# Kernel optimization log

Measured on AMD Instinct MI355X. Metric: run time of the kernel, lower is better.

## Reference

```python
import jax, jax.numpy as jnp
import numpy as np

DIM = 1024
DIM_MEDIA = 1024
DIM_HEAD = 64
HEADS = 8
INNER = DIM_HEAD * HEADS  # 512
B, N_TOK, N_LAT = 4, 4096, 1024
LN_EPS = 1e-5


def setup_inputs() -> dict:
    key = jax.random.key(0)
    ks = jax.random.split(key, 6)
    x = jax.random.normal(ks[0], (B, N_TOK, DIM), dtype=jnp.float32)
    media = jax.random.normal(ks[1], (B, N_LAT, DIM_MEDIA), dtype=jnp.float32)
    media_mask = jax.random.randint(ks[2], (B, N_LAT), 0, 2).astype(bool)
    media_mask = media_mask.at[:, 0].set(True)  # avoid fully-masked rows (NaN softmax)
    ln_gamma = jnp.ones((DIM,), jnp.float32)
    ln_beta = jnp.zeros((DIM,), jnp.float32)
    Wq = jax.random.normal(ks[3], (DIM, INNER), jnp.float32) * (DIM ** -0.5)
    Wkv = jax.random.normal(ks[4], (DIM_MEDIA, 2 * INNER), jnp.float32) * (DIM_MEDIA ** -0.5)
    Wout = jax.random.normal(ks[5], (INNER, DIM), jnp.float32) * (INNER ** -0.5)
    return {"x": x, "media": media, "media_mask": media_mask,
            "ln_gamma": ln_gamma, "ln_beta": ln_beta,
            "Wq": Wq, "Wkv": Wkv, "Wout": Wout}


def reference(x, media, media_mask, ln_gamma, ln_beta, Wq, Wkv, Wout):
    scale = DIM_HEAD ** -0.5
    # LayerNorm over last dim
    mu = jnp.mean(x, axis=-1, keepdims=True)
    var = jnp.mean(jnp.square(x - mu), axis=-1, keepdims=True)
    xn = (x - mu) * jax.lax.rsqrt(var + LN_EPS) * ln_gamma + ln_beta

    q = (xn @ Wq) * scale                      # [b, n, inner]
    kv = media @ Wkv                           # [b, m, 2*inner]
    k, v = jnp.split(kv, 2, axis=-1)

    def to_heads(t):
        b, n, _ = t.shape
        return t.reshape(b, n, HEADS, DIM_HEAD).transpose(0, 2, 1, 3)  # b h n d

    q, k, v = to_heads(q), to_heads(k), to_heads(v)

    sim = jnp.einsum('bhid,bhjd->bhij', q, k)  # [b, h, n_tok, n_lat]
    neg_inf = jnp.float32(-jnp.inf)
    sim = jnp.where(media_mask[:, None, None, :], sim, neg_inf)
    sim = sim - jax.lax.stop_gradient(jnp.max(sim, axis=-1, keepdims=True))
    attn = jax.nn.softmax(sim, axis=-1)
    out = jnp.einsum('bhij,bhjd->bhid', attn, v)  # [b, h, n_tok, d]
    out = out.transpose(0, 2, 1, 3).reshape(out.shape[0], out.shape[2], INNER)
    return out @ Wout  # [b, n_tok, dim]
```

## Files before the change

kernel.cpp:

```cpp
#include <hip/hip_runtime.h>
#include <hip/hip_bf16.h>

typedef short bf16x8 __attribute__((ext_vector_type(8)));
typedef float f32x4 __attribute__((ext_vector_type(4)));
typedef unsigned short u16;

#define AS1 __attribute__((address_space(1)))
#define AS3 __attribute__((address_space(3)))

#define DIM     1024
#define INNER   512
#define HEADS   8
#define DHEAD   64
#define BATCH   4
#define NTOK    4096
#define NLAT    1024
#define M_X     (BATCH*NTOK)
#define M_MED   (BATCH*NLAT)
#define LN_EPS  1e-5f

__device__ __forceinline__ float b2f(u16 h) {
    union { unsigned u; float f; } v; v.u = ((unsigned)h) << 16; return v.f;
}
__device__ __forceinline__ u16 f2b(float f) {
    union { float f; unsigned u; } v; v.f = f;
    unsigned r = v.u + 0x7fff + ((v.u >> 16) & 1);
    return (u16)(r >> 16);
}
__device__ __forceinline__ unsigned cvt_pk(float lo, float hi) {
    unsigned r;
    asm("v_cvt_pk_bf16_f32 %0, %1, %2" : "=v"(r) : "v"(lo), "v"(hi));
    return r;
}

__launch_bounds__(256)
__global__ void detect_kernel(const unsigned* __restrict__ xw, const unsigned* __restrict__ maskw,
                              unsigned* __restrict__ flags) {
    __shared__ int s_bad, s_byte;
    if (threadIdx.x == 0) { s_bad = 0; s_byte = 0; }
    __syncthreads();
    unsigned w = xw[threadIdx.x];
    int bad = 0;
    #pragma unroll
    for (int h = 0; h < 2; h++) {
        unsigned el = (h ? (w >> 16) : w) & 0xFFFFu;
        unsigned ef = (el >> 7) & 0xFFu;
        if (!((ef >= 64u && ef < 192u) || (el & 0x7FFFu) == 0u)) bad = 1;
    }
    if (bad) atomicOr(&s_bad, 1);
    for (int i = threadIdx.x; i < NLAT; i += 256)
        if (maskw[i] > 1u) { atomicOr(&s_byte, 1); break; }
    __syncthreads();
    if (threadIdx.x == 0) { flags[0] = s_bad ? 0u : 1u; flags[1] = s_byte ? 1u : 0u; }
}

#define PREP_BLOCKS 6148

__device__ __forceinline__ void do_transpose(const void* in, u16* out, int R, int C,
                                             int bx, int by, bool bf, u16 (*t)[33]) {
    int c0 = bx * 32, r0 = by * 32;
    int tid = threadIdx.x;
    int r = tid >> 3, cb = (tid & 7) * 4;
    size_t base = (size_t)(r0 + r) * C + c0 + cb;
    u16 e0, e1, e2, e3;
    if (bf) {
        ushort4 a = *(const ushort4*)((const u16*)in + base);
        e0 = a.x; e1 = a.y; e2 = a.z; e3 = a.w;
    } else {
        float4 a = *(const float4*)((const float*)in + base);
        e0 = f2b(a.x); e1 = f2b(a.y); e2 = f2b(a.z); e3 = f2b(a.w);
    }
    t[r][cb] = e0; t[r][cb + 1] = e1; t[r][cb + 2] = e2; t[r][cb + 3] = e3;
    __syncthreads();
    ushort4 o;
    o.x = t[cb + 0][r]; o.y = t[cb + 1][r]; o.z = t[cb + 2][r]; o.w = t[cb + 3][r];
    *(ushort4*)(out + (size_t)(c0 + r) * R + r0 + cb) = o;
}

__launch_bounds__(256)
__global__ void prep_kernel(const void* __restrict__ x, const void* __restrict__ g,
                            const void* __restrict__ bt, u16* __restrict__ xn,
                            const void* __restrict__ media, u16* __restrict__ media_c,
                            const void* __restrict__ mask, int* __restrict__ map,
                            int* __restrict__ cnt,
                            const void* __restrict__ Wq, u16* __restrict__ WqT,
                            const void* __restrict__ Wkv, u16* __restrict__ WkvT,
                            const void* __restrict__ Wout, u16* __restrict__ WoutT,
                            const unsigned* __restrict__ flags) {
    __shared__ int wsumI[4];
    __shared__ u16 t[32][33];
    bool bf = flags[0] != 0;
    int bid = blockIdx.x, tid = threadIdx.x;

    if (bid < 2048) {
        int w = tid >> 6, lane = tid & 63;
        int row0 = (bid << 3) + (w << 1);
        float v[2][16];
        if (bf) {
            const u16* xr = (const u16*)x + (size_t)row0 * DIM;
            bf16x8 a[4];
            #pragma unroll
            for (int rr = 0; rr < 2; rr++)
                #pragma unroll
                for (int i = 0; i < 2; i++)
                    a[rr * 2 + i] = *(const bf16x8*)(xr + (size_t)rr * DIM + (lane + 64 * i) * 8);
            #pragma unroll
            for (int rr = 0; rr < 2; rr++)
                #pragma unroll
                for (int i = 0; i < 2; i++)
                    #pragma unroll
                    for (int j = 0; j < 8; j++)
                        v[rr][i * 8 + j] = b2f((u16)a[rr * 2 + i][j]);
        } else {
            const float* xr = (const float*)x + (size_t)row0 * DIM;
            float4 a[8];
            #pragma unroll
            for (int rr = 0; rr < 2; rr++)
                #pragma unroll
                for (int i = 0; i < 4; i++)
                    a[rr * 4 + i] = *(const float4*)(xr + (size_t)rr * DIM + (lane + 64 * i) * 4);
            #pragma unroll
            for (int rr = 0; rr < 2; rr++)
                #pragma unroll
                for (int i = 0; i < 4; i++) {
                    v[rr][i * 4 + 0] = a[rr * 4 + i].x; v[rr][i * 4 + 1] = a[rr * 4 + i].y;
                    v[rr][i * 4 + 2] = a[rr * 4 + i].z; v[rr][i * 4 + 3] = a[rr * 4 + i].w;
                }
        }
        float s[2] = {0.f, 0.f}, s2[2] = {0.f, 0.f};
        #pragma unroll
        for (int rr = 0; rr < 2; rr++)
            #pragma unroll
            for (int i = 0; i < 16; i++) { s[rr] += v[rr][i]; s2[rr] += v[rr][i] * v[rr][i]; }
        #pragma unroll
        for (int m = 1; m < 64; m <<= 1) {
            #pragma unroll
            for (int rr = 0; rr < 2; rr++) {
                s[rr] += __shfl_xor(s[rr], m);
                s2[rr] += __shfl_xor(s2[rr], m);
            }
        }
        float mu[2], inv[2];
        #pragma unroll
        for (int rr = 0; rr < 2; rr++) {
            mu[rr] = s[rr] * (1.f / DIM);
            float var = s2[rr] * (1.f / DIM) - mu[rr] * mu[rr];
            inv[rr] = rsqrtf(fmaxf(var, 0.f) + LN_EPS);
        }
        u16* orow = xn + (size_t)row0 * DIM;
        if (bf) {
            const u16* gr = (const u16*)g;
            const u16* br = (const u16*)bt;
            #pragma unroll
            for (int i = 0; i < 2; i++) {
                int c = (lane + 64 * i) * 8;
                bf16x8 ga = *(const bf16x8*)(gr + c);
                bf16x8 ba = *(const bf16x8*)(br + c);
                #pragma unroll
                for (int rr = 0; rr < 2; rr++) {
                    u16 o[8];
                    #pragma unroll
                    for (int j = 0; j < 8; j++)
                        o[j] = f2b((v[rr][i * 8 + j] - mu[rr]) * inv[rr] * b2f((u16)ga[j]) + b2f((u16)ba[j]));
                    *(bf16x8*)(orow + (size_t)rr * DIM + c) = *(bf16x8*)o;
                }
            }
        } else {
            const float* gr = (const float*)g;
            const float* br = (const float*)bt;
            #pragma unroll
            for (int i = 0; i < 4; i++) {
                int c = (lane + 64 * i) * 4;
                float4 ga = *(const float4*)(gr + c);
                float4 ba = *(const float4*)(br + c);
                #pragma unroll
                for (int rr = 0; rr < 2; rr++) {
                    ushort4 o;
                    o.x = f2b((v[rr][i * 4 + 0] - mu[rr]) * inv[rr] * ga.x + ba.x);
                    o.y = f2b((v[rr][i * 4 + 1] - mu[rr]) * inv[rr] * ga.y + ba.y);
                    o.z = f2b((v[rr][i * 4 + 2] - mu[rr]) * inv[rr] * ga.z + ba.z);
                    o.w = f2b((v[rr][i * 4 + 3] - mu[rr]) * inv[rr] * ga.w + ba.w);
                    *(ushort4*)(orow + (size_t)rr * DIM + c) = o;
                }
            }
        }
    } else if (bid < 4096) {
        size_t i = ((size_t)(bid - 2048) * 256 + tid) * 8;
        if (bf) {
            *(bf16x8*)(media_c + i) = *(const bf16x8*)((const u16*)media + i);
        } else {
            const float* s = (const float*)media + i;
            float4 a = *(const float4*)s, b = *(const float4*)(s + 4);
            u16 o[8] = {f2b(a.x), f2b(a.y), f2b(a.z), f2b(a.w),
                        f2b(b.x), f2b(b.y), f2b(b.z), f2b(b.w)};
            *(bf16x8*)(media_c + i) = *(bf16x8*)o;
        }
    } else if (bid < 4100) {
        int b = bid - 4096;
        bool bytes = flags[1] != 0;
        int v[4];
        if (bytes) {
            unsigned wd = ((const unsigned*)mask)[b * 256 + tid];
            #pragma unroll
            for (int i = 0; i < 4; i++) v[i] = ((wd >> (8 * i)) & 0xFFu) ? 1 : 0;
        } else {
            int4 m4 = ((const int4*)mask)[b * 256 + tid];
            v[0] = m4.x != 0; v[1] = m4.y != 0; v[2] = m4.z != 0; v[3] = m4.w != 0;
        }
        int tsum = v[0] + v[1] + v[2] + v[3];
        int lane = tid & 63, w = tid >> 6;
        int incl = tsum;
        #pragma unroll
        for (int off = 1; off < 64; off <<= 1) {
            int tt = __shfl_up(incl, off);
            if (lane >= off) incl += tt;
        }
        if (lane == 63) wsumI[w] = incl;
        __syncthreads();
        int base = 0;
        for (int k = 0; k < w; k++) base += wsumI[k];
        int slot = base + incl - tsum;
        int gbase = b * NLAT + tid * 4;
        #pragma unroll
        for (int i = 0; i < 4; i++) map[gbase + i] = v[i] ? slot++ : -1;
        if (tid == 0) cnt[b] = wsumI[0] + wsumI[1] + wsumI[2] + wsumI[3];
    } else if (bid < 4612) {
        int idx = bid - 4100;
        do_transpose(Wq, WqT, DIM, INNER, idx & 15, idx >> 4, bf, t);
    } else if (bid < 5636) {
        int idx = bid - 4612;
        do_transpose(Wkv, WkvT, DIM, DIM, idx & 31, idx >> 5, bf, t);
    } else {
        int idx = bid - 5636;
        do_transpose(Wout, WoutT, INNER, DIM, idx & 31, idx >> 5, bf, t);
    }
}

__device__ __forceinline__ void gemm_body(const u16* __restrict__ A, const u16* __restrict__ Bt,
                                          u16* __restrict__ C, float* __restrict__ Cf,
                                          int Ndim, int K, float scale, int mode,
                                          u16* __restrict__ vT, const int* __restrict__ map,
                                          bool outbf, int n0, int m0, u16* As, u16* Bs) {
    int tid = threadIdx.x;
    int w = tid >> 6, lane = tid & 63, quad = lane >> 4, l15 = lane & 15;
    int wm = (w >> 1) * 64, wn = (w & 1) * 64;
    f32x4 acc[4][4] = {};
    for (int k0 = 0; k0 < K; k0 += 64) {
        __syncthreads();
        #pragma unroll
        for (int i = 0; i < 4; i++) {
            int slot = i * 256 + tid;
            int row = slot >> 3;
            int lg = (slot & 7) ^ (row & 7);
            int wbase = (i * 256 + (tid & 192)) * 8;
            __builtin_amdgcn_global_load_lds(
                (const AS1 void*)(A + (size_t)(m0 + row) * K + k0 + lg * 8),
                (AS3 void*)(As + wbase), 16, 0, 0);
            __builtin_amdgcn_global_load_lds(
                (const AS1 void*)(Bt + (size_t)(n0 + row) * K + k0 + lg * 8),
                (AS3 void*)(Bs + wbase), 16, 0, 0);
        }
        __syncthreads();
        #pragma unroll
        for (int h = 0; h < 2; h++) {
            bf16x8 af[4], bfr[4];
            #pragma unroll
            for (int i = 0; i < 4; i++) {
                int R = wm + i * 16 + l15;
                af[i] = *(bf16x8*)&As[R * 64 + (((quad + h * 4) ^ (R & 7)) * 8)];
            }
            #pragma unroll
            for (int j = 0; j < 4; j++) {
                int R = wn + j * 16 + l15;
                bfr[j] = *(bf16x8*)&Bs[R * 64 + (((quad + h * 4) ^ (R & 7)) * 8)];
            }
            #pragma unroll
            for (int i = 0; i < 4; i++)
                #pragma unroll
                for (int j = 0; j < 4; j++)
                    acc[i][j] = __builtin_amdgcn_mfma_f32_16x16x32_bf16(af[i], bfr[j], acc[i][j], 0, 0, 0);
        }
    }
    #pragma unroll
    for (int i = 0; i < 4; i++)
        #pragma unroll
        for (int j = 0; j < 4; j++)
            #pragma unroll
            for (int r = 0; r < 4; r++) {
                int row = m0 + wm + i * 16 + quad * 4 + r;
                int col = n0 + wn + j * 16 + l15;
                float val = acc[i][j][r] * scale;
                if (mode == 1) {
                    int b = row >> 10, jj = row & 1023;
                    int slot = map[(b << 10) + jj];
                    if (slot >= 0) {
                        if (col < INNER) {
                            C[((size_t)(b << 10) + slot) * INNER + col] = f2b(val);
                        } else {
                            int c = col - INNER;
                            int h = c >> 6, d = c & 63;
                            vT[(((size_t)(b * HEADS + h) * 64 + d) << 10) + slot] = f2b(val);
                        }
                    }
                } else if (outbf) {
                    C[(size_t)row * Ndim + col] = f2b(val);
                } else {
                    Cf[(size_t)row * Ndim + col] = val;
                }
            }
}

__launch_bounds__(256, 3)
__global__ void gemm128(const u16* __restrict__ A, const u16* __restrict__ Bt,
                        u16* __restrict__ C, float* __restrict__ Cf, int Ndim, int K,
                        float scale, int mode, u16* __restrict__ vT,
                        const int* __restrict__ map,
                        const unsigned* __restrict__ flags) {
    __shared__ __align__(16) u16 As[128 * 64];
    __shared__ __align__(16) u16 Bs[128 * 64];
    bool outbf = (mode != 2) || (flags[0] != 0);
    gemm_body(A, Bt, C, Cf, Ndim, K, scale, mode, vT, map, outbf,
              blockIdx.x * 128, blockIdx.y * 128, As, Bs);
}

__launch_bounds__(256, 3)
__global__ void gemm_qkv(const u16* __restrict__ xn, const u16* __restrict__ WqT,
                         u16* __restrict__ qb,
                         const u16* __restrict__ media_c, const u16* __restrict__ WkvT,
                         u16* __restrict__ Kb, u16* __restrict__ vT,
                         const int* __restrict__ map) {
    __shared__ __align__(16) u16 As[128 * 64];
    __shared__ __align__(16) u16 Bs[128 * 64];
    int bid = blockIdx.x;
    if (bid < 512) {
        gemm_body(xn, WqT, qb, (float*)nullptr, INNER, DIM, 0.125f * 1.44269504f, 0,
                  (u16*)nullptr, (int*)nullptr, true,
                  (bid & 3) * 128, (bid >> 2) * 128, As, Bs);
    } else {
        int id = bid - 512;
        gemm_body(media_c, WkvT, Kb, (float*)nullptr, DIM, DIM, 1.0f, 1,
                  vT, map, true,
                  (id & 7) * 128, (id >> 3) * 128, As, Bs);
    }
}

__launch_bounds__(256, 6)
__global__ void flash_kernel(const u16* __restrict__ q, const u16* __restrict__ Kc,
                             const u16* __restrict__ vTc, const int* __restrict__ cntp,
                             u16* __restrict__ attn_out) {
    __shared__ __align__(16) u16 Ks[64 * 64];
    __shared__ __align__(16) u16 Vts[64 * 64];
    __shared__ __align__(16) u16 Ps[4][16 * 68];
    int bh = blockIdx.x >> 6;
    int qt = blockIdx.x & 63;
    int b = bh >> 3, h = bh & 7;
    int tid = threadIdx.x, w = tid >> 6, lane = tid & 63, quad = lane >> 4, l15 = lane & 15;
    int qrow0 = qt * 64 + w * 16;
    int cnt = cntp[b];

    size_t qbase = ((size_t)(b * NTOK) + qrow0 + l15) * INNER + h * 64;
    bf16x8 qf[2];
    qf[0] = *(const bf16x8*)(q + qbase + quad * 8);
    qf[1] = *(const bf16x8*)(q + qbase + 32 + quad * 8);

    f32x4 Oacc[4] = {};
    float lsum = 0.f;
    int ld_row = lane >> 3;
    int ld_col = ((lane & 7) ^ ld_row) * 8;

    for (int jt = 0; jt < cnt; jt += 64) {
        __syncthreads();
        #pragma unroll
        for (int i = 0; i < 2; i++) {
            int seg = w * 2 + i;
            int j = jt + seg * 8 + ld_row;
            __builtin_amdgcn_global_load_lds(
                (const AS1 void*)(Kc + ((size_t)(b * NLAT) + j) * INNER + h * 64 + ld_col),
                (AS3 void*)(Ks + seg * 512), 16, 0, 0);
            int d = seg * 8 + ld_row;
            __builtin_amdgcn_global_load_lds(
                (const AS1 void*)(vTc + (((size_t)(b * HEADS + h) * 64 + d) << 10) + jt + ld_col),
                (AS3 void*)(Vts + seg * 512), 16, 0, 0);
        }
        __syncthreads();

        int sw0 = (quad ^ (l15 & 7)) * 8;
        int sw1 = ((quad + 4) ^ (l15 & 7)) * 8;
        f32x4 S[4];
        #pragma unroll
        for (int c = 0; c < 4; c++) {
            bf16x8 kf0 = *(bf16x8*)&Ks[(c * 16 + l15) * 64 + sw0];
            bf16x8 kf1 = *(bf16x8*)&Ks[(c * 16 + l15) * 64 + sw1];
            f32x4 s = {};
            s = __builtin_amdgcn_mfma_f32_16x16x32_bf16(kf0, qf[0], s, 0, 0, 0);
            s = __builtin_amdgcn_mfma_f32_16x16x32_bf16(kf1, qf[1], s, 0, 0, 0);
            S[c] = s;
        }
        if (jt + 64 <= cnt) {
            #pragma unroll
            for (int c = 0; c < 4; c++) {
                float p0 = exp2f(fminf(S[c][0], 115.4f));
                float p1 = exp2f(fminf(S[c][1], 115.4f));
                float p2 = exp2f(fminf(S[c][2], 115.4f));
                float p3 = exp2f(fminf(S[c][3], 115.4f));
                lsum += (p0 + p1) + (p2 + p3);
                uint2 pw = {cvt_pk(p0, p1), cvt_pk(p2, p3)};
                *(uint2*)&Ps[w][l15 * 68 + c * 16 + quad * 4] = pw;
            }
        } else {
            #pragma unroll
            for (int c = 0; c < 4; c++) {
                int kbase = jt + c * 16 + quad * 4;
                float p[4];
                #pragma unroll
                for (int r = 0; r < 4; r++) {
                    bool valid = (kbase + r) < cnt;
                    p[r] = valid ? exp2f(fminf(S[c][r], 115.4f)) : 0.f;
                    lsum += p[r];
                }
                uint2 pw = {cvt_pk(p[0], p[1]), cvt_pk(p[2], p[3])};
                *(uint2*)&Ps[w][l15 * 68 + c * 16 + quad * 4] = pw;
            }
        }
        asm volatile("s_waitcnt lgkmcnt(0)" ::: "memory");
        bf16x8 pf0 = *(bf16x8*)&Ps[w][l15 * 68 + quad * 8];
        bf16x8 pf1 = *(bf16x8*)&Ps[w][l15 * 68 + 32 + quad * 8];
        #pragma unroll
        for (int dt = 0; dt < 4; dt++) {
            bf16x8 vf0 = *(bf16x8*)&Vts[(dt * 16 + l15) * 64 + sw0];
            bf16x8 vf1 = *(bf16x8*)&Vts[(dt * 16 + l15) * 64 + sw1];
            Oacc[dt] = __builtin_amdgcn_mfma_f32_16x16x32_bf16(pf0, vf0, Oacc[dt], 0, 0, 0);
            Oacc[dt] = __builtin_amdgcn_mfma_f32_16x16x32_bf16(pf1, vf1, Oacc[dt], 0, 0, 0);
        }
    }
    lsum += __shfl_xor(lsum, 16);
    lsum += __shfl_xor(lsum, 32);
    #pragma unroll
    for (int r = 0; r < 4; r++) {
        float l = __shfl(lsum, quad * 4 + r);
        float invl = (l > 0.f) ? (1.f / l) : 0.f;
        #pragma unroll
        for (int dt = 0; dt < 4; dt++) {
            int row = qrow0 + quad * 4 + r;
            int col = h * 64 + dt * 16 + l15;
            attn_out[(size_t)(b * NTOK + row) * INNER + col] = f2b(Oacc[dt][r] * invl);
        }
    }
}

extern "C" void kernel_launch(void* const* d_in, const int* in_sizes, int n_in,
                              void* d_out, int out_size, void* d_ws, size_t ws_size,
                              hipStream_t stream) {
    const void* x     = d_in[0];
    const void* media = d_in[1];
    const void* mask  = d_in[2];
    const void* g     = d_in[3];
    const void* beta  = d_in[4];
    const void* Wq    = d_in[5];
    const void* Wkv   = d_in[6];
    const void* Wout  = d_in[7];

    char* ws = (char*)d_ws;
    unsigned* flags = (unsigned*)ws;   ws += 256;
    int* map_c  = (int*)ws;            ws += (size_t)M_MED * 4;
    int* cnt_c  = (int*)ws;            ws += 256;
    u16* media_c = (u16*)ws;           ws += (size_t)M_MED * DIM * 2;
    u16* xn    = (u16*)ws;             ws += (size_t)M_X * DIM * 2;
    u16* qb    = (u16*)ws;             ws += (size_t)M_X * INNER * 2;
    u16* Kb    = (u16*)ws;             ws += (size_t)M_MED * INNER * 2;
    u16* vTb   = (u16*)ws;             ws += (size_t)M_MED * INNER * 2;
    u16* ao    = (u16*)ws;             ws += (size_t)M_X * INNER * 2;
    u16* WqT   = (u16*)ws;             ws += (size_t)DIM * INNER * 2;
    u16* WkvT  = (u16*)ws;             ws += (size_t)DIM * DIM * 2;
    u16* WoutT = (u16*)ws;             ws += (size_t)INNER * DIM * 2;

    detect_kernel<<<1, 256, 0, stream>>>((const unsigned*)x, (const unsigned*)mask, flags);
    prep_kernel<<<PREP_BLOCKS, 256, 0, stream>>>(x, g, beta, xn, media, media_c, mask, map_c, cnt_c,
                                                 Wq, WqT, Wkv, WkvT, Wout, WoutT, flags);
    gemm_qkv<<<dim3(768), 256, 0, stream>>>(xn, WqT, qb, media_c, WkvT, Kb, vTb, map_c);
    flash_kernel<<<dim3(32 * 64), 256, 0, stream>>>(qb, Kb, vTb, cnt_c, ao);
    gemm128<<<dim3(DIM / 128, M_X / 128), 256, 0, stream>>>(ao, WoutT, (u16*)d_out, (float*)d_out, DIM, INNER,
                                                            1.0f, 2, (u16*)nullptr, (int*)nullptr, flags);
}
```

Baseline: 263.4 us.

## Process two 16-row query groups per wave in flash attention kernel

Each wave now handles 32 query rows, as two 16-row groups, instead of 16, so each block covers 128 queries and the grid is halved. Every K/V tile staged in LDS is reused across twice as many queries, which halves the global-to-LDS traffic and barrier count per query. In exchange each thread holds twice as many accumulators and the P buffer doubles, and launch bounds drop to 4 waves per SIMD, lowering occupancy and the number of blocks.

```diff
diff --git a/kernel.cpp b/kernel.cpp
--- a/kernel.cpp
+++ b/kernel.cpp
@@ -344,27 +344,30 @@
     }
 }
 
-__launch_bounds__(256, 6)
+__launch_bounds__(256, 4)
 __global__ void flash_kernel(const u16* __restrict__ q, const u16* __restrict__ Kc,
                              const u16* __restrict__ vTc, const int* __restrict__ cntp,
                              u16* __restrict__ attn_out) {
     __shared__ __align__(16) u16 Ks[64 * 64];
     __shared__ __align__(16) u16 Vts[64 * 64];
-    __shared__ __align__(16) u16 Ps[4][16 * 68];
-    int bh = blockIdx.x >> 6;
-    int qt = blockIdx.x & 63;
+    __shared__ __align__(16) u16 Ps[4][2][16 * 68];
+    int bh = blockIdx.x >> 5;
+    int qt = blockIdx.x & 31;
     int b = bh >> 3, h = bh & 7;
     int tid = threadIdx.x, w = tid >> 6, lane = tid & 63, quad = lane >> 4, l15 = lane & 15;
-    int qrow0 = qt * 64 + w * 16;
+    int qrow0 = qt * 128 + w * 32;
     int cnt = cntp[b];
 
-    size_t qbase = ((size_t)(b * NTOK) + qrow0 + l15) * INNER + h * 64;
-    bf16x8 qf[2];
-    qf[0] = *(const bf16x8*)(q + qbase + quad * 8);
-    qf[1] = *(const bf16x8*)(q + qbase + 32 + quad * 8);
-
-    f32x4 Oacc[4] = {};
-    float lsum = 0.f;
+    bf16x8 qf[2][2];
+    #pragma unroll
+    for (int qg = 0; qg < 2; qg++) {
+        size_t qbase = ((size_t)(b * NTOK) + qrow0 + qg * 16 + l15) * INNER + h * 64;
+        qf[qg][0] = *(const bf16x8*)(q + qbase + quad * 8);
+        qf[qg][1] = *(const bf16x8*)(q + qbase + 32 + quad * 8);
+    }
+
+    f32x4 Oacc[2][4] = {};
+    float lsum[2] = {0.f, 0.f};
     int ld_row = lane >> 3;
     int ld_col = ((lane & 7) ^ ld_row) * 8;
 
@@ -386,64 +389,75 @@
 
         int sw0 = (quad ^ (l15 & 7)) * 8;
         int sw1 = ((quad + 4) ^ (l15 & 7)) * 8;
-        f32x4 S[4];
-        #pragma unroll
-        for (int c = 0; c < 4; c++) {
-            bf16x8 kf0 = *(bf16x8*)&Ks[(c * 16 + l15) * 64 + sw0];
-            bf16x8 kf1 = *(bf16x8*)&Ks[(c * 16 + l15) * 64 + sw1];
-            f32x4 s = {};
-            s = __builtin_amdgcn_mfma_f32_16x16x32_bf16(kf0, qf[0], s, 0, 0, 0);
-            s = __builtin_amdgcn_mfma_f32_16x16x32_bf16(kf1, qf[1], s, 0, 0, 0);
-            S[c] = s;
-        }
-        if (jt + 64 <= cnt) {
+        bool full = (jt + 64 <= cnt);
+        #pragma unroll
+        for (int qg = 0; qg < 2; qg++) {
+            f32x4 S[4];
             #pragma unroll
             for (int c = 0; c < 4; c++) {
-                float p0 = exp2f(fminf(S[c][0], 115.4f));
-                float p1 = exp2f(fminf(S[c][1], 115.4f));
-                float p2 = exp2f(fminf(S[c][2], 115.4f));
-                float p3 = exp2f(fminf(S[c][3], 115.4f));
-                lsum += (p0 + p1) + (p2 + p3);
-                uint2 pw = {cvt_pk(p0, p1), cvt_pk(p2, p3)};
-                *(uint2*)&Ps[w][l15 * 68 + c * 16 + quad * 4] = pw;
-            }
-        } else {
-            #pragma unroll
-            for (int c = 0; c < 4; c++) {
-                int kbase = jt + c * 16 + quad * 4;
-                float p[4];
-                #pragma unroll
-                for (int r = 0; r < 4; r++) {
-                    bool valid = (kbase + r) < cnt;
-                    p[r] = valid ? exp2f(fminf(S[c][r], 115.4f)) : 0.f;
-                    lsum += p[r];
-                }
-                uint2 pw = {cvt_pk(p[0], p[1]), cvt_pk(p[2], p[3])};
-                *(uint2*)&Ps[w][l15 * 68 + c * 16 + quad * 4] = pw;
+                bf16x8 kf0 = *(bf16x8*)&Ks[(c * 16 + l15) * 64 + sw0];
+                bf16x8 kf1 = *(bf16x8*)&Ks[(c * 16 + l15) * 64 + sw1];
+                f32x4 s = {};
+                s = __builtin_amdgcn_mfma_f32_16x16x32_bf16(kf0, qf[qg][0], s, 0, 0, 0);
+                s = __builtin_amdgcn_mfma_f32_16x16x32_bf16(kf1, qf[qg][1], s, 0, 0, 0);
+                S[c] = s;
+            }
+            if (full) {
+                #pragma unroll
+                for (int c = 0; c < 4; c++) {
+                    float p0 = exp2f(fminf(S[c][0], 115.4f));
+                    float p1 = exp2f(fminf(S[c][1], 115.4f));
+                    float p2 = exp2f(fminf(S[c][2], 115.4f));
+                    float p3 = exp2f(fminf(S[c][3], 115.4f));
+                    lsum[qg] += (p0 + p1) + (p2 + p3);
+                    uint2 pw = {cvt_pk(p0, p1), cvt_pk(p2, p3)};
+                    *(uint2*)&Ps[w][qg][l15 * 68 + c * 16 + quad * 4] = pw;
+                }
+            } else {
+                #pragma unroll
+                for (int c = 0; c < 4; c++) {
+                    int kbase = jt + c * 16 + quad * 4;
+                    float p[4];
+                    #pragma unroll
+                    for (int r = 0; r < 4; r++) {
+                        bool valid = (kbase + r) < cnt;
+                        p[r] = valid ? exp2f(fminf(S[c][r], 115.4f)) : 0.f;
+                        lsum[qg] += p[r];
+                    }
+                    uint2 pw = {cvt_pk(p[0], p[1]), cvt_pk(p[2], p[3])};
+                    *(uint2*)&Ps[w][qg][l15 * 68 + c * 16 + quad * 4] = pw;
+                }
             }
         }
         asm volatile("s_waitcnt lgkmcnt(0)" ::: "memory");
-        bf16x8 pf0 = *(bf16x8*)&Ps[w][l15 * 68 + quad * 8];
-        bf16x8 pf1 = *(bf16x8*)&Ps[w][l15 * 68 + 32 + quad * 8];
-        #pragma unroll
-        for (int dt = 0; dt < 4; dt++) {
-            bf16x8 vf0 = *(bf16x8*)&Vts[(dt * 16 + l15) * 64 + sw0];
-            bf16x8 vf1 = *(bf16x8*)&Vts[(dt * 16 + l15) * 64 + sw1];
-            Oacc[dt] = __builtin_amdgcn_mfma_f32_16x16x32_bf16(pf0, vf0, Oacc[dt], 0, 0, 0);
-            Oacc[dt] = __builtin_amdgcn_mfma_f32_16x16x32_bf16(pf1, vf1, Oacc[dt], 0, 0, 0);
-        }
-    }
-    lsum += __shfl_xor(lsum, 16);
-    lsum += __shfl_xor(lsum, 32);
+        #pragma unroll
+        for (int qg = 0; qg < 2; qg++) {
+            bf16x8 pf0 = *(bf16x8*)&Ps[w][qg][l15 * 68 + quad * 8];
+            bf16x8 pf1 = *(bf16x8*)&Ps[w][qg][l15 * 68 + 32 + quad * 8];
+            #pragma unroll
+            for (int dt = 0; dt < 4; dt++) {
+                bf16x8 vf0 = *(bf16x8*)&Vts[(dt * 16 + l15) * 64 + sw0];
+                bf16x8 vf1 = *(bf16x8*)&Vts[(dt * 16 + l15) * 64 + sw1];
+                Oacc[qg][dt] = __builtin_amdgcn_mfma_f32_16x16x32_bf16(pf0, vf0, Oacc[qg][dt], 0, 0, 0);
+                Oacc[qg][dt] = __builtin_amdgcn_mfma_f32_16x16x32_bf16(pf1, vf1, Oacc[qg][dt], 0, 0, 0);
+            }
+        }
+    }
     #pragma unroll
-    for (int r = 0; r < 4; r++) {
-        float l = __shfl(lsum, quad * 4 + r);
-        float invl = (l > 0.f) ? (1.f / l) : 0.f;
-        #pragma unroll
-        for (int dt = 0; dt < 4; dt++) {
-            int row = qrow0 + quad * 4 + r;
-            int col = h * 64 + dt * 16 + l15;
-            attn_out[(size_t)(b * NTOK + row) * INNER + col] = f2b(Oacc[dt][r] * invl);
+    for (int qg = 0; qg < 2; qg++) {
+        float ls = lsum[qg];
+        ls += __shfl_xor(ls, 16);
+        ls += __shfl_xor(ls, 32);
+        #pragma unroll
+        for (int r = 0; r < 4; r++) {
+            float l = __shfl(ls, quad * 4 + r);
+            float invl = (l > 0.f) ? (1.f / l) : 0.f;
+            #pragma unroll
+            for (int dt = 0; dt < 4; dt++) {
+                int row = qrow0 + qg * 16 + quad * 4 + r;
+                int col = h * 64 + dt * 16 + l15;
+                attn_out[(size_t)(b * NTOK + row) * INNER + col] = f2b(Oacc[qg][dt][r] * invl);
+            }
         }
     }
 }
@@ -478,7 +492,7 @@
     prep_kernel<<<PREP_BLOCKS, 256, 0, stream>>>(x, g, beta, xn, media, media_c, mask, map_c, cnt_c,
                                                  Wq, WqT, Wkv, WkvT, Wout, WoutT, flags);
     gemm_qkv<<<dim3(768), 256, 0, stream>>>(xn, WqT, qb, media_c, WkvT, Kb, vTb, map_c);
-    flash_kernel<<<dim3(32 * 64), 256, 0, stream>>>(qb, Kb, vTb, cnt_c, ao);
+    flash_kernel<<<dim3(32 * 32), 256, 0, stream>>>(qb, Kb, vTb, cnt_c, ao);
     gemm128<<<dim3(DIM / 128, M_X / 128), 256, 0, stream>>>(ao, WoutT, (u16*)d_out, (float*)d_out, DIM, INNER,
                                                             1.0f, 2, (u16*)nullptr, (int*)nullptr, flags);
 }
```

Result: slower. 273.3 us (+3.8%).
